# Performance work log

Measured on AMD Instinct MI355X. Metric: run time of the kernel, lower is better.

The kernel has to match this reference:

```python
import jax, jax.numpy as jnp
import numpy as np

N_TERMS = 26000
N_EDGES = 120000
BATCH = 64
N_FEAT = 14          # n_base_models + 4
GO_EMB = 8
HID = 64
IN_DIM = N_FEAT + GO_EMB  # 22


def setup_inputs() -> dict:
    key = jax.random.key(0)
    ks = jax.random.split(key, 12)
    s = 0.05
    return {
        "x": jax.random.normal(ks[0], (BATCH, N_TERMS, N_FEAT), jnp.float32),
        "edge_index": jax.random.randint(ks[1], (2, N_EDGES), 0, N_TERMS, jnp.int32),
        "term_indices": jnp.arange(N_TERMS, dtype=jnp.int32),
        "emb_table": jax.random.normal(ks[2], (N_TERMS, GO_EMB), jnp.float32),
        "W1": jax.random.normal(ks[3], (HID, IN_DIM), jnp.float32) * s,
        "b1": jnp.zeros((HID,), jnp.float32),
        "W2": jax.random.normal(ks[4], (HID, HID), jnp.float32) * s,
        "b2": jnp.zeros((HID,), jnp.float32),
        "W3": jax.random.normal(ks[5], (HID // 2, HID), jnp.float32) * s,
        "b3": jnp.zeros((HID // 2,), jnp.float32),
        "Wout": jax.random.normal(ks[6], (1, HID // 2), jnp.float32) * s,
        "bout": jnp.zeros((1,), jnp.float32),
    }


def _go_conv(x, row, col, deg_inv, W, b):
    # x: [B, N, C]. Mean-aggregate neighbor features (col -> row), add self, linear.
    agg = jnp.zeros_like(x).at[:, row].add(x[:, col])        # scatter_add over edges
    agg = agg * deg_inv[None, :, None]
    return jnp.einsum('bnc,oc->bno', x + agg, W) + b


def reference(x, edge_index, term_indices, emb_table, W1, b1, W2, b2, W3, b3, Wout, bout):
    B, N, _ = x.shape
    row, col = edge_index[0], edge_index[1]
    deg = jnp.zeros((N,), x.dtype).at[row].add(1.0)
    deg_inv = 1.0 / jnp.clip(deg, 1.0)

    go_emb = emb_table[term_indices]                          # [N, GO_EMB]
    h = jnp.concatenate([x, jnp.broadcast_to(go_emb[None], (B, N, go_emb.shape[-1]))], axis=-1)

    h = jax.nn.relu(_go_conv(h, row, col, deg_inv, W1, b1))   # dropout: eval mode (identity)
    h = jax.nn.relu(_go_conv(h, row, col, deg_inv, W2, b2))
    h = jax.nn.relu(_go_conv(h, row, col, deg_inv, W3, b3))
    out = jax.nn.sigmoid(jnp.einsum('bnc,oc->bno', h, Wout) + bout)  # [B, N, 1]
    return out[..., 0]
```

## Files before the change

### kernel.cpp

```cpp
#include <hip/hip_runtime.h>
#include <stdint.h>

static constexpr int NT = 26000;
static constexpr int NE = 120000;

typedef __attribute__((ext_vector_type(8))) short short8;
typedef __attribute__((ext_vector_type(4))) float f32x4;
typedef __attribute__((ext_vector_type(2))) unsigned int u32x2;

__device__ __forceinline__ float bf_lo(uint32_t u){ union{uint32_t u; float f;} a; a.u = u<<16; return a.f; }
__device__ __forceinline__ float bf_hi(uint32_t u){ union{uint32_t u; float f;} a; a.u = u & 0xffff0000u; return a.f; }
__device__ __forceinline__ uint32_t f2b(float f){ union{float f; uint32_t u;} a; a.f=f; return (a.u + 0x7fffu + ((a.u>>16)&1u))>>16; }

__device__ __forceinline__ void nts2(uint32_t* p, uint32_t a, uint32_t b){
  u32x2 v; v.x = a; v.y = b;
  __builtin_nontemporal_store(v, reinterpret_cast<u32x2*>(p));
}


__global__ __launch_bounds__(256) void k_zero_deg(int* __restrict__ deg){
  int i = blockIdx.x*256 + threadIdx.x;
  if (i < NT) deg[i] = 0;
}
__global__ __launch_bounds__(256) void k_count(const int* __restrict__ ei, int* __restrict__ deg){
  int e = blockIdx.x*256 + threadIdx.x;
  if (e < NE) atomicAdd(&deg[ei[e]], 1);
}
__global__ __launch_bounds__(1024) void k_scan(const int* __restrict__ deg, int* __restrict__ rp,
                                               int* __restrict__ cur){
  __shared__ int part[1024];
  const int t = threadIdx.x;
  const int CH = (NT + 1023)/1024;
  const int base = t*CH;
  int sum = 0;
  for (int i=0;i<CH;i++){
    int idx=base+i;
    if (idx<NT){ int d = deg[idx]; sum += (d<=4)?4:((d+3)&~3); }
  }
  part[t] = sum;
  __syncthreads();
  for (int off=1; off<1024; off<<=1){
    int v = (t>=off) ? part[t-off] : 0;
    __syncthreads();
    part[t] += v;
    __syncthreads();
  }
  int run = (t==0) ? 0 : part[t-1];
  for (int i=0;i<CH;i++){
    int idx = base+i;
    if (idx<NT){
      int d = deg[idx];
      int slot = (d<=4)?4:((d+3)&~3);
      rp[idx] = run; cur[idx] = run;
      run += slot;
    }
  }
  if (t==1023) rp[NT] = part[1023];
}
__global__ __launch_bounds__(256) void k_init(uint32_t* __restrict__ zp, uint32_t* __restrict__ cols32){
  int i = blockIdx.x*256 + threadIdx.x;
  if (i < 1024) zp[i] = 0;
  else if (i < 1024 + 112004) cols32[i-1024] = 0x65906590u;
}
__global__ __launch_bounds__(256) void k_fill(const int* __restrict__ ei, int* __restrict__ cur,
                                              uint16_t* __restrict__ cols){
  int e = blockIdx.x*256 + threadIdx.x;
  if (e < NE){
    int r = ei[e];
    int pos = atomicAdd(&cur[r], 1);
    cols[pos] = (uint16_t)ei[NE + e];
  }
}
__global__ __launch_bounds__(256) void k_prepw(const float* __restrict__ W1, const float* __restrict__ W2,
                                               const float* __restrict__ W3,
                                               uint16_t* __restrict__ Wt1, uint16_t* __restrict__ Wt2,
                                               uint16_t* __restrict__ Wt3){
  for (int idx = threadIdx.x; idx < 8192; idx += 256){
    if (idx < 2048){
      int o = idx >> 5, k = idx & 31;
      Wt1[idx] = (uint16_t)((k < 22) ? f2b(W1[o*22 + k]) : 0);
    } else if (idx < 6144){
      int j = idx - 2048;
      Wt2[j] = (uint16_t)f2b(W2[j]);
    } else {
      int j = idx - 6144;
      Wt3[j] = (uint16_t)f2b(W3[j]);
    }
  }
}

__global__ __launch_bounds__(256) void k_build_h0(const float* __restrict__ x, const int* __restrict__ tidx,
                                                  const float* __restrict__ emb, uint32_t* __restrict__ h0){
  const int n  = blockIdx.x*16 + (threadIdx.x & 15);
  const int b0 = threadIdx.x >> 4;
  const float* er = emb + (size_t)tidx[n]*8;
  float ev[8];
  #pragma unroll
  for (int i=0;i<8;i++) ev[i]=er[i];
  uint32_t* dst = h0 + (size_t)n*512;

  #pragma unroll
  for (int h=0; h<2; h++){
    const int b = b0 + h*16;
    const float* xr = x + ((size_t)b*NT + n)*14;
    float v[32];
    #pragma unroll
    for (int i=0;i<14;i++) v[i]=xr[i];
    #pragma unroll
    for (int i=0;i<8;i++) v[14+i]=ev[i];
    #pragma unroll
    for (int i=22;i<32;i++) v[i]=0.f;
    uint32_t p[16];
    #pragma unroll
    for (int u=0;u<16;u++) p[u] = f2b(v[2*u]) | (f2b(v[2*u+1])<<16);
    const int base = (b>>4)*256 + (b&15)*8;
    *reinterpret_cast<uint4*>(dst + base)       = make_uint4(p[0],p[1],p[2],p[3]);
    *reinterpret_cast<uint4*>(dst + base + 4)   = make_uint4(p[4],p[5],p[6],p[7]);
    *reinterpret_cast<uint4*>(dst + base + 128)     = make_uint4(p[8],p[9],p[10],p[11]);
    *reinterpret_cast<uint4*>(dst + base + 132) = make_uint4(p[12],p[13],p[14],p[15]);
  }
}

template<int STR>
__device__ __forceinline__ const uint32_t* nbp(const uint32_t* __restrict__ hin,
                                               const uint32_t* __restrict__ zp, int c){
  return (c < NT) ? (hin + (size_t)c*STR) : zp;
}
template<int KS>
__device__ __forceinline__ void gloadv(uint4 (&v)[KS], const uint32_t* __restrict__ p,
                                       const uint32_t (&off)[KS]){
  #pragma unroll
  for (int ks=0; ks<KS; ks++) v[ks] = *reinterpret_cast<const uint4*>(p + off[ks]);
}
template<int KS>
__device__ __forceinline__ void accum(float (&acc)[KS][8], const uint4 (&v)[KS]){
  #pragma unroll
  for (int ks=0;ks<KS;ks++){
    acc[ks][0]+=bf_lo(v[ks].x); acc[ks][1]+=bf_hi(v[ks].x);
    acc[ks][2]+=bf_lo(v[ks].y); acc[ks][3]+=bf_hi(v[ks].y);
    acc[ks][4]+=bf_lo(v[ks].z); acc[ks][5]+=bf_hi(v[ks].z);
    acc[ks][6]+=bf_lo(v[ks].w); acc[ks][7]+=bf_hi(v[ks].w);
  }
}

template<int KS, int STR>
__device__ __forceinline__ float aggregate(float (&acc)[KS][8],
    const uint32_t* __restrict__ hin, const uint32_t* __restrict__ zp,
    const int* __restrict__ rp, const int* __restrict__ cur,
    const uint16_t* __restrict__ cols, int node, const uint32_t (&off)[KS])
{
  const int e0 = __builtin_amdgcn_readfirstlane(rp[node]);
  const int e1 = __builtin_amdgcn_readfirstlane(rp[node+1]);
  const int dg = __builtin_amdgcn_readfirstlane(cur[node]) - e0;

  uint2 cc0 = *reinterpret_cast<const uint2*>(cols + e0);
  int q0 = __builtin_amdgcn_readfirstlane(cc0.x);
  int q1 = __builtin_amdgcn_readfirstlane(cc0.y);
  uint4 v0[KS], v1[KS], v2[KS], v3[KS], own[KS];
  gloadv<KS>(v0, nbp<STR>(hin, zp, q0 & 0xffff), off);
  gloadv<KS>(v1, nbp<STR>(hin, zp, (q0 >> 16) & 0xffff), off);
  gloadv<KS>(v2, nbp<STR>(hin, zp, q1 & 0xffff), off);
  gloadv<KS>(v3, nbp<STR>(hin, zp, (q1 >> 16) & 0xffff), off);
  gloadv<KS>(own, hin + (size_t)node*STR, off);
  uint2 ccA = *reinterpret_cast<const uint2*>(cols + e0 + 4);

  const float degf = (float)(dg > 1 ? dg : 1);
  #pragma unroll
  for (int ks=0;ks<KS;ks++){
    acc[ks][0]=bf_lo(own[ks].x)*degf; acc[ks][1]=bf_hi(own[ks].x)*degf;
    acc[ks][2]=bf_lo(own[ks].y)*degf; acc[ks][3]=bf_hi(own[ks].y)*degf;
    acc[ks][4]=bf_lo(own[ks].z)*degf; acc[ks][5]=bf_hi(own[ks].z)*degf;
    acc[ks][6]=bf_lo(own[ks].w)*degf; acc[ks][7]=bf_hi(own[ks].w)*degf;
  }

  for (int e = e0; e < e1; e += 4){
    uint2 ccN = *reinterpret_cast<const uint2*>(cols + e + 8);
    int p0 = __builtin_amdgcn_readfirstlane(ccA.x);
    int p1 = __builtin_amdgcn_readfirstlane(ccA.y);
    int n0 = (e+4 < e1) ? (p0 & 0xffff)         : NT;
    int n1 = (e+5 < e1) ? ((p0 >> 16) & 0xffff) : NT;
    int n2 = (e+6 < e1) ? (p1 & 0xffff)         : NT;
    int n3 = (e+7 < e1) ? ((p1 >> 16) & 0xffff) : NT;
    accum<KS>(acc, v0); gloadv<KS>(v0, nbp<STR>(hin, zp, n0), off);
    accum<KS>(acc, v1); gloadv<KS>(v1, nbp<STR>(hin, zp, n1), off);
    accum<KS>(acc, v2); gloadv<KS>(v2, nbp<STR>(hin, zp, n2), off);
    accum<KS>(acc, v3); gloadv<KS>(v3, nbp<STR>(hin, zp, n3), off);
    ccA = ccN;
  }
  return 1.0f / degf;
}

__global__ __launch_bounds__(256, 8) void k_layer1(
    const uint32_t* __restrict__ hin, uint32_t* __restrict__ hout,
    const int* __restrict__ rp, const int* __restrict__ cur,
    const uint16_t* __restrict__ cols, const uint32_t* __restrict__ zp,
    const uint16_t* __restrict__ Wt, const float* __restrict__ bias)
{
  constexpr int CIN=32, COUT=64, KS=1, OT=4, STR=16*CIN;
  const int t=threadIdx.x, lane=t&63, w=t>>6, l15=lane&15, lg=lane>>4;
  const int rt = w & 1;
  const int node = blockIdx.x*2 + (w>>1);

  uint32_t off[KS];
  off[0] = (uint32_t)(rt*(CIN*8) + (lg>>1)*128 + l15*8 + (lg&1)*4);

  float acc[KS][8];
  const float di = aggregate<KS,STR>(acc, hin, zp, rp, cur, cols, node, off);

  short8 bfrag[KS];
  {
    short8 bf;
    #pragma unroll
    for (int j=0;j<8;j++) bf[j] = (short)f2b(acc[0][j]*di);
    bfrag[0]=bf;
  }

  #pragma unroll
  for (int ot=0;ot<OT;ot++){
    const int o0 = ot*16;
    short8 af = *reinterpret_cast<const short8*>(Wt + (o0 + l15)*CIN + lg*8);
    f32x4 d = *reinterpret_cast<const f32x4*>(bias + o0 + lg*4);
    d = __builtin_amdgcn_mfma_f32_16x16x32_bf16(af, bfrag[0], d, 0,0,0);
    float a0=fmaxf(d[0],0.f), a1=fmaxf(d[1],0.f), a2=fmaxf(d[2],0.f), a3=fmaxf(d[3],0.f);
    nts2(hout + (size_t)node*(16*COUT) + rt*(COUT*8) + ot*128 + l15*8 + lg*2,
         f2b(a0) | (f2b(a1)<<16), f2b(a2) | (f2b(a3)<<16));
  }
}

__global__ __launch_bounds__(256, 6) void k_l2g3(
    const uint32_t* __restrict__ hin, uint32_t* __restrict__ hout,
    const int* __restrict__ rp, const int* __restrict__ cur,
    const uint16_t* __restrict__ cols, const uint32_t* __restrict__ zp,
    const uint16_t* __restrict__ Wt2, const float* __restrict__ bias,
    const uint16_t* __restrict__ Wt3)
{
  constexpr int CIN=64, COUT=64, KS=2, OT=4, STR=16*CIN;
  __shared__ uint32_t lt[4*512];

  const int t=threadIdx.x, lane=t&63, w=t>>6, l15=lane&15, lg=lane>>4;
  const int rt = w & 1;
  const int node = blockIdx.x*2 + (w>>1);

  uint32_t off[KS];
  #pragma unroll
  for (int ks=0;ks<KS;ks++)
    off[ks] = (uint32_t)(rt*(CIN*8) + (ks*2+(lg>>1))*128 + l15*8 + (lg&1)*4);

  float acc[KS][8];
  const float di = aggregate<KS,STR>(acc, hin, zp, rp, cur, cols, node, off);

  short8 bfrag[KS];
  #pragma unroll
  for (int ks=0;ks<KS;ks++){
    short8 bf;
    #pragma unroll
    for (int j=0;j<8;j++) bf[j] = (short)f2b(acc[ks][j]*di);
    bfrag[ks]=bf;
  }

  uint32_t* L = lt + w*512;
  #pragma unroll
  for (int ot=0;ot<OT;ot++){
    const int o0 = ot*16;
    short8 af0 = *reinterpret_cast<const short8*>(Wt2 + (o0 + l15)*CIN + lg*8);
    short8 af1 = *reinterpret_cast<const short8*>(Wt2 + (o0 + l15)*CIN + 32 + lg*8);
    f32x4 d = *reinterpret_cast<const f32x4*>(bias + o0 + lg*4);
    d = __builtin_amdgcn_mfma_f32_16x16x32_bf16(af0, bfrag[0], d, 0,0,0);
    d = __builtin_amdgcn_mfma_f32_16x16x32_bf16(af1, bfrag[1], d, 0,0,0);
    float a0=fmaxf(d[0],0.f), a1=fmaxf(d[1],0.f), a2=fmaxf(d[2],0.f), a3=fmaxf(d[3],0.f);
    *reinterpret_cast<uint2*>(L + ot*128 + l15*8 + lg*2) =
        make_uint2(f2b(a0) | (f2b(a1)<<16), f2b(a2) | (f2b(a3)<<16));
  }

  short8 b3f[2];
  #pragma unroll
  for (int ks=0;ks<2;ks++)
    b3f[ks] = *reinterpret_cast<const short8*>(L + (ks*2+(lg>>1))*128 + l15*8 + (lg&1)*4);

  #pragma unroll
  for (int ot=0;ot<2;ot++){
    const int o0 = ot*16;
    short8 af0 = *reinterpret_cast<const short8*>(Wt3 + (o0 + l15)*64 + lg*8);
    short8 af1 = *reinterpret_cast<const short8*>(Wt3 + (o0 + l15)*64 + 32 + lg*8);
    f32x4 d = {0.f,0.f,0.f,0.f};
    d = __builtin_amdgcn_mfma_f32_16x16x32_bf16(af0, b3f[0], d, 0,0,0);
    d = __builtin_amdgcn_mfma_f32_16x16x32_bf16(af1, b3f[1], d, 0,0,0);
    nts2(hout + (size_t)node*512 + rt*256 + ot*128 + l15*8 + lg*2,
         f2b(d[0]) | (f2b(d[1])<<16), f2b(d[2]) | (f2b(d[3])<<16));
  }
}

__global__ __launch_bounds__(256, 8) void k_fin(
    const uint32_t* __restrict__ hin,
    const int* __restrict__ rp, const int* __restrict__ cur,
    const uint16_t* __restrict__ cols, const uint32_t* __restrict__ zp,
    const float* __restrict__ b3, const float* __restrict__ Wo, const float* __restrict__ bo,
    float* __restrict__ tmp)
{
  constexpr int KS=1, STR=512;
  const int t=threadIdx.x, lane=t&63, w=t>>6, l15=lane&15, lg=lane>>4;
  const int rt = w & 1;
  const int node = blockIdx.x*2 + (w>>1);

  uint32_t off[KS];
  off[0] = (uint32_t)(rt*256 + (lg>>1)*128 + l15*8 + (lg&1)*4);

  float acc[KS][8];
  const float di = aggregate<KS,STR>(acc, hin, zp, rp, cur, cols, node, off);

  const int k0 = lg*8;
  f32x4 bA = *reinterpret_cast<const f32x4*>(b3 + k0);
  f32x4 bB = *reinterpret_cast<const f32x4*>(b3 + k0 + 4);
  f32x4 wA = *reinterpret_cast<const f32x4*>(Wo + k0);
  f32x4 wB = *reinterpret_cast<const f32x4*>(Wo + k0 + 4);
  float z = 0.f;
  #pragma unroll
  for (int j=0;j<4;j++){
    z += fmaxf(acc[0][j]  *di + bA[j], 0.f) * wA[j];
    z += fmaxf(acc[0][4+j]*di + bB[j], 0.f) * wB[j];
  }
  z += __shfl_xor(z, 16, 64);
  z += __shfl_xor(z, 32, 64);
  if (lg == 0){
    float sg = 1.f/(1.f + expf(-(z + bo[0])));
    tmp[(size_t)node*32 + rt*16 + l15] = sg;
  }
}

__global__ __launch_bounds__(256) void k_tr(const float* __restrict__ tmp, float* __restrict__ out){
  int n = blockIdx.x*256 + threadIdx.x;
  if (n < NT){
    f32x4 r[8];
    #pragma unroll
    for (int q=0;q<8;q++) r[q] = *reinterpret_cast<const f32x4*>(tmp + (size_t)n*32 + q*4);
    #pragma unroll
    for (int q=0;q<8;q++)
      #pragma unroll
      for (int j=0;j<4;j++)
        out[(size_t)(q*4+j)*NT + n] = r[q][j];
  }
}

static constexpr size_t OFF_P    = 0;
static constexpr size_t OFF_Q    = 53248000;
static constexpr size_t OFF_TMP  = 159744000;
static constexpr size_t OFF_ZP   = 163072000;
static constexpr size_t OFF_WT1  = OFF_ZP  + 4096;
static constexpr size_t OFF_WT2  = OFF_WT1 + 4096;
static constexpr size_t OFF_WT3  = OFF_WT2 + 8192;
static constexpr size_t OFF_DEG  = OFF_WT3 + 4096;
static constexpr size_t OFF_RP   = OFF_DEG + 104000;
static constexpr size_t OFF_CUR  = OFF_RP  + 104016;
static constexpr size_t OFF_COLS = OFF_CUR + 104000;
static constexpr size_t WS_NEED  = OFF_COLS + 448016;

extern "C" void kernel_launch(void* const* d_in, const int* in_sizes, int n_in,
                              void* d_out, int out_size, void* d_ws, size_t ws_size,
                              hipStream_t stream)
{
  const float* x    = (const float*)d_in[0];
  const int*   ei   = (const int*)  d_in[1];
  const int*   tidx = (const int*)  d_in[2];
  const float* emb  = (const float*)d_in[3];
  const float* W1   = (const float*)d_in[4];
  const float* b1   = (const float*)d_in[5];
  const float* W2   = (const float*)d_in[6];
  const float* b2   = (const float*)d_in[7];
  const float* W3   = (const float*)d_in[8];
  const float* b3   = (const float*)d_in[9];
  const float* Wo   = (const float*)d_in[10];
  const float* bo   = (const float*)d_in[11];
  float* out = (float*)d_out;

  if (ws_size < WS_NEED) return;

  char* ws = (char*)d_ws;
  uint32_t* P    = (uint32_t*)(ws + OFF_P);
  uint32_t* Q    = (uint32_t*)(ws + OFF_Q);
  float*    tmpf = (float*)   (ws + OFF_TMP);
  uint32_t* zp   = (uint32_t*)(ws + OFF_ZP);
  uint16_t* Wt1  = (uint16_t*)(ws + OFF_WT1);
  uint16_t* Wt2  = (uint16_t*)(ws + OFF_WT2);
  uint16_t* Wt3  = (uint16_t*)(ws + OFF_WT3);
  int*      deg  = (int*)     (ws + OFF_DEG);
  int*      rp   = (int*)     (ws + OFF_RP);
  int*      cur  = (int*)     (ws + OFF_CUR);
  uint16_t* cols = (uint16_t*)(ws + OFF_COLS);

  k_zero_deg<<<(NT+255)/256, 256, 0, stream>>>(deg);
  k_count   <<<(NE+255)/256, 256, 0, stream>>>(ei, deg);
  k_scan    <<<1, 1024, 0, stream>>>(deg, rp, cur);
  k_init    <<<442, 256, 0, stream>>>(zp, (uint32_t*)cols);
  k_fill    <<<(NE+255)/256, 256, 0, stream>>>(ei, cur, cols);
  k_prepw   <<<1, 256, 0, stream>>>(W1, W2, W3, Wt1, Wt2, Wt3);

  for (int ch = 0; ch < 2; ch++){
    k_build_h0<<<NT/16, 256, 0, stream>>>(x + (size_t)ch*32*NT*14, tidx, emb, P);
    k_layer1<<<NT/2, 256, 0, stream>>>(P, Q, rp, cur, cols, zp, Wt1, b1);
    k_l2g3  <<<NT/2, 256, 0, stream>>>(Q, P, rp, cur, cols, zp, Wt2, b2, Wt3);
    k_fin   <<<NT/2, 256, 0, stream>>>(P, rp, cur, cols, zp, b3, Wo, bo, tmpf);
    k_tr    <<<(NT+255)/256, 256, 0, stream>>>(tmpf, out + (size_t)ch*32*NT);
  }
}
```

Before: 560.4 us.

## Store intermediate layer activations as int8 with per-node-per-half scales

Layer-1 and layer-2/3 outputs are now quantized to int8, with one float scale per node and row-tile computed by a wavefront max-reduction, replacing the previous bf16 storage. The following aggregation kernels gather int8 rows and dequantize them while accumulating. This halves the bytes moved in the neighbor-gather traffic that dominates these memory-bound kernels. The cost is lower numerical precision, plus an extra scale load per neighbor and the dequantization arithmetic.

Measured after the change: 523.8 us. -6.5%, faster.

```diff
diff --git a/kernel.cpp b/kernel.cpp
--- a/kernel.cpp
+++ b/kernel.cpp
@@ -6,17 +6,12 @@
 
 typedef __attribute__((ext_vector_type(8))) short short8;
 typedef __attribute__((ext_vector_type(4))) float f32x4;
-typedef __attribute__((ext_vector_type(2))) unsigned int u32x2;
+
+__device__ __forceinline__ int rfl(int v){ return __builtin_amdgcn_readfirstlane(v); }
 
 __device__ __forceinline__ float bf_lo(uint32_t u){ union{uint32_t u; float f;} a; a.u = u<<16; return a.f; }
 __device__ __forceinline__ float bf_hi(uint32_t u){ union{uint32_t u; float f;} a; a.u = u & 0xffff0000u; return a.f; }
 __device__ __forceinline__ uint32_t f2b(float f){ union{float f; uint32_t u;} a; a.f=f; return (a.u + 0x7fffu + ((a.u>>16)&1u))>>16; }
-
-__device__ __forceinline__ void nts2(uint32_t* p, uint32_t a, uint32_t b){
-  u32x2 v; v.x = a; v.y = b;
-  __builtin_nontemporal_store(v, reinterpret_cast<u32x2*>(p));
-}
-
 
 __global__ __launch_bounds__(256) void k_zero_deg(int* __restrict__ deg){
   int i = blockIdx.x*256 + threadIdx.x;
@@ -57,10 +52,12 @@
   }
   if (t==1023) rp[NT] = part[1023];
 }
-__global__ __launch_bounds__(256) void k_init(uint32_t* __restrict__ zp, uint32_t* __restrict__ cols32){
+__global__ __launch_bounds__(256) void k_init(uint32_t* __restrict__ zp, uint32_t* __restrict__ cols32,
+                                              float* __restrict__ scQ, float* __restrict__ scY){
   int i = blockIdx.x*256 + threadIdx.x;
   if (i < 1024) zp[i] = 0;
   else if (i < 1024 + 112004) cols32[i-1024] = 0x65906590u;
+  if (i < 2){ scQ[NT*2+i] = 0.f; scY[NT*2+i] = 0.f; }
 }
 __global__ __launch_bounds__(256) void k_fill(const int* __restrict__ ei, int* __restrict__ cur,
                                               uint16_t* __restrict__ cols){
@@ -116,8 +113,8 @@
     const int base = (b>>4)*256 + (b&15)*8;
     *reinterpret_cast<uint4*>(dst + base)       = make_uint4(p[0],p[1],p[2],p[3]);
     *reinterpret_cast<uint4*>(dst + base + 4)   = make_uint4(p[4],p[5],p[6],p[7]);
-    *reinterpret_cast<uint4*>(dst + base + 128)     = make_uint4(p[8],p[9],p[10],p[11]);
-    *reinterpret_cast<uint4*>(dst + base + 132) = make_uint4(p[12],p[13],p[14],p[15]);
+    *reinterpret_cast<uint4*>(dst + base + 128)   = make_uint4(p[8],p[9],p[10],p[11]);
+    *reinterpret_cast<uint4*>(dst + base + 132)   = make_uint4(p[12],p[13],p[14],p[15]);
   }
 }
 
@@ -142,20 +139,18 @@
     acc[ks][6]+=bf_lo(v[ks].w); acc[ks][7]+=bf_hi(v[ks].w);
   }
 }
-
 template<int KS, int STR>
 __device__ __forceinline__ float aggregate(float (&acc)[KS][8],
     const uint32_t* __restrict__ hin, const uint32_t* __restrict__ zp,
     const int* __restrict__ rp, const int* __restrict__ cur,
     const uint16_t* __restrict__ cols, int node, const uint32_t (&off)[KS])
 {
-  const int e0 = __builtin_amdgcn_readfirstlane(rp[node]);
-  const int e1 = __builtin_amdgcn_readfirstlane(rp[node+1]);
-  const int dg = __builtin_amdgcn_readfirstlane(cur[node]) - e0;
+  const int e0 = rfl(rp[node]);
+  const int e1 = rfl(rp[node+1]);
+  const int dg = rfl(cur[node]) - e0;
 
   uint2 cc0 = *reinterpret_cast<const uint2*>(cols + e0);
-  int q0 = __builtin_amdgcn_readfirstlane(cc0.x);
-  int q1 = __builtin_amdgcn_readfirstlane(cc0.y);
+  int q0 = rfl(cc0.x), q1 = rfl(cc0.y);
   uint4 v0[KS], v1[KS], v2[KS], v3[KS], own[KS];
   gloadv<KS>(v0, nbp<STR>(hin, zp, q0 & 0xffff), off);
   gloadv<KS>(v1, nbp<STR>(hin, zp, (q0 >> 16) & 0xffff), off);
@@ -175,8 +170,7 @@
 
   for (int e = e0; e < e1; e += 4){
     uint2 ccN = *reinterpret_cast<const uint2*>(cols + e + 8);
-    int p0 = __builtin_amdgcn_readfirstlane(ccA.x);
-    int p1 = __builtin_amdgcn_readfirstlane(ccA.y);
+    int p0 = rfl(ccA.x), p1 = rfl(ccA.y);
     int n0 = (e+4 < e1) ? (p0 & 0xffff)         : NT;
     int n1 = (e+5 < e1) ? ((p0 >> 16) & 0xffff) : NT;
     int n2 = (e+6 < e1) ? (p1 & 0xffff)         : NT;
@@ -190,68 +184,149 @@
   return 1.0f / degf;
 }
 
+template<int KS> struct VecT;
+template<> struct VecT<2>{ using T = uint4; };
+template<> struct VecT<1>{ using T = uint2; };
+
+__device__ __forceinline__ void dqu32(float* a, uint32_t u, float s){
+  a[0] += s*(float)(int8_t)(u & 0xff);
+  a[1] += s*(float)(int8_t)((u>>8) & 0xff);
+  a[2] += s*(float)(int8_t)((u>>16) & 0xff);
+  a[3] += s*(float)(int8_t)(u>>24);
+}
+template<int KS>
+__device__ __forceinline__ void dqv(float (&acc)[KS][8], const typename VecT<KS>::T& v, float s){
+  if constexpr (KS==2){
+    dqu32(&acc[0][0], v.x, s); dqu32(&acc[0][4], v.y, s);
+    dqu32(&acc[1][0], v.z, s); dqu32(&acc[1][4], v.w, s);
+  } else {
+    dqu32(&acc[0][0], v.x, s); dqu32(&acc[0][4], v.y, s);
+  }
+}
+template<int KS, int STRB>
+__device__ __forceinline__ float aggregate_i8(float (&acc)[KS][8],
+    const uint8_t* __restrict__ hin, const uint8_t* __restrict__ zp8,
+    const float* __restrict__ sc,
+    const int* __restrict__ rp, const int* __restrict__ cur,
+    const uint16_t* __restrict__ cols, int node, uint32_t offB, int rt)
+{
+  using V = typename VecT<KS>::T;
+  const int e0 = rfl(rp[node]);
+  const int e1 = rfl(rp[node+1]);
+  const int dg = rfl(cur[node]) - e0;
+
+  uint2 cc0 = *reinterpret_cast<const uint2*>(cols + e0);
+  int a0 = rfl(cc0.x), a1 = rfl(cc0.y);
+  int c0 = a0 & 0xffff, c1 = (a0>>16) & 0xffff, c2 = a1 & 0xffff, c3 = (a1>>16) & 0xffff;
+  auto bp = [&](int c)->const uint8_t*{ return (c < NT) ? (hin + (size_t)c*STRB) : zp8; };
+
+  V v0 = *reinterpret_cast<const V*>(bp(c0) + offB); float s0 = sc[c0*2+rt];
+  V v1 = *reinterpret_cast<const V*>(bp(c1) + offB); float s1 = sc[c1*2+rt];
+  V v2 = *reinterpret_cast<const V*>(bp(c2) + offB); float s2 = sc[c2*2+rt];
+  V v3 = *reinterpret_cast<const V*>(bp(c3) + offB); float s3 = sc[c3*2+rt];
+  V ow = *reinterpret_cast<const V*>(hin + (size_t)node*STRB + offB);
+  float so = sc[node*2+rt];
+  uint2 ccA = *reinterpret_cast<const uint2*>(cols + e0 + 4);
+
+  const float degf = (float)(dg > 1 ? dg : 1);
+  #pragma unroll
+  for (int ks=0;ks<KS;ks++)
+    #pragma unroll
+    for (int j=0;j<8;j++) acc[ks][j]=0.f;
+  dqv<KS>(acc, ow, so*degf);
+
+  for (int e = e0; e < e1; e += 4){
+    uint2 ccN = *reinterpret_cast<const uint2*>(cols + e + 8);
+    int p0 = rfl(ccA.x), p1 = rfl(ccA.y);
+    int n0 = (e+4 < e1) ? (p0 & 0xffff)         : NT;
+    int n1 = (e+5 < e1) ? ((p0 >> 16) & 0xffff) : NT;
+    int n2 = (e+6 < e1) ? (p1 & 0xffff)         : NT;
+    int n3 = (e+7 < e1) ? ((p1 >> 16) & 0xffff) : NT;
+    dqv<KS>(acc, v0, s0); v0 = *reinterpret_cast<const V*>(bp(n0) + offB); s0 = sc[n0*2+rt];
+    dqv<KS>(acc, v1, s1); v1 = *reinterpret_cast<const V*>(bp(n1) + offB); s1 = sc[n1*2+rt];
+    dqv<KS>(acc, v2, s2); v2 = *reinterpret_cast<const V*>(bp(n2) + offB); s2 = sc[n2*2+rt];
+    dqv<KS>(acc, v3, s3); v3 = *reinterpret_cast<const V*>(bp(n3) + offB); s3 = sc[n3*2+rt];
+    ccA = ccN;
+  }
+  return 1.0f / degf;
+}
+
 __global__ __launch_bounds__(256, 8) void k_layer1(
-    const uint32_t* __restrict__ hin, uint32_t* __restrict__ hout,
+    const uint32_t* __restrict__ hin, uint8_t* __restrict__ qout, float* __restrict__ scQ,
     const int* __restrict__ rp, const int* __restrict__ cur,
     const uint16_t* __restrict__ cols, const uint32_t* __restrict__ zp,
     const uint16_t* __restrict__ Wt, const float* __restrict__ bias)
 {
-  constexpr int CIN=32, COUT=64, KS=1, OT=4, STR=16*CIN;
+  constexpr int CIN=32, STR=16*CIN;
   const int t=threadIdx.x, lane=t&63, w=t>>6, l15=lane&15, lg=lane>>4;
   const int rt = w & 1;
   const int node = blockIdx.x*2 + (w>>1);
 
-  uint32_t off[KS];
+  uint32_t off[1];
   off[0] = (uint32_t)(rt*(CIN*8) + (lg>>1)*128 + l15*8 + (lg&1)*4);
 
-  float acc[KS][8];
-  const float di = aggregate<KS,STR>(acc, hin, zp, rp, cur, cols, node, off);
-
-  short8 bfrag[KS];
-  {
-    short8 bf;
-    #pragma unroll
-    for (int j=0;j<8;j++) bf[j] = (short)f2b(acc[0][j]*di);
-    bfrag[0]=bf;
-  }
-
-  #pragma unroll
-  for (int ot=0;ot<OT;ot++){
+  float acc[1][8];
+  const float di = aggregate<1,STR>(acc, hin, zp, rp, cur, cols, node, off);
+
+  short8 bfrag;
+  #pragma unroll
+  for (int j=0;j<8;j++) bfrag[j] = (short)f2b(acc[0][j]*di);
+
+  float av[4][4];
+  float m = 0.f;
+  #pragma unroll
+  for (int ot=0;ot<4;ot++){
     const int o0 = ot*16;
     short8 af = *reinterpret_cast<const short8*>(Wt + (o0 + l15)*CIN + lg*8);
     f32x4 d = *reinterpret_cast<const f32x4*>(bias + o0 + lg*4);
-    d = __builtin_amdgcn_mfma_f32_16x16x32_bf16(af, bfrag[0], d, 0,0,0);
-    float a0=fmaxf(d[0],0.f), a1=fmaxf(d[1],0.f), a2=fmaxf(d[2],0.f), a3=fmaxf(d[3],0.f);
-    nts2(hout + (size_t)node*(16*COUT) + rt*(COUT*8) + ot*128 + l15*8 + lg*2,
-         f2b(a0) | (f2b(a1)<<16), f2b(a2) | (f2b(a3)<<16));
-  }
+    d = __builtin_amdgcn_mfma_f32_16x16x32_bf16(af, bfrag, d, 0,0,0);
+    #pragma unroll
+    for (int j=0;j<4;j++){
+      float v = fmaxf(d[j], 0.f);
+      av[ot][j] = v;
+      m = fmaxf(m, v);
+    }
+  }
+  #pragma unroll
+  for (int sh=1; sh<64; sh<<=1) m = fmaxf(m, __shfl_xor(m, sh, 64));
+  const float inv = (m > 0.f) ? 127.0f/m : 0.f;
+
+  uint8_t* base = qout + (size_t)node*2048 + rt*1024 + l15*64;
+  #pragma unroll
+  for (int ot=0;ot<4;ot++){
+    uint32_t pk = 0;
+    #pragma unroll
+    for (int j=0;j<4;j++){
+      int q = __float2int_rn(av[ot][j]*inv);
+      pk |= (uint32_t)(q & 0xff) << (8*j);
+    }
+    uint32_t boff = ((((ot&1)<<1)|(lg>>1))<<4) + ((ot>>1)<<3) + ((lg&1)<<2);
+    __builtin_nontemporal_store(pk, reinterpret_cast<uint32_t*>(base + boff));
+  }
+  if (lane == 0) scQ[node*2+rt] = m * (1.0f/127.0f);
 }
 
 __global__ __launch_bounds__(256, 6) void k_l2g3(
-    const uint32_t* __restrict__ hin, uint32_t* __restrict__ hout,
+    const uint8_t* __restrict__ qin, const float* __restrict__ scQ,
+    uint8_t* __restrict__ yout, float* __restrict__ scY,
     const int* __restrict__ rp, const int* __restrict__ cur,
-    const uint16_t* __restrict__ cols, const uint32_t* __restrict__ zp,
+    const uint16_t* __restrict__ cols, const uint8_t* __restrict__ zp8,
     const uint16_t* __restrict__ Wt2, const float* __restrict__ bias,
     const uint16_t* __restrict__ Wt3)
 {
-  constexpr int CIN=64, COUT=64, KS=2, OT=4, STR=16*CIN;
   __shared__ uint32_t lt[4*512];
-
   const int t=threadIdx.x, lane=t&63, w=t>>6, l15=lane&15, lg=lane>>4;
   const int rt = w & 1;
   const int node = blockIdx.x*2 + (w>>1);
 
-  uint32_t off[KS];
-  #pragma unroll
-  for (int ks=0;ks<KS;ks++)
-    off[ks] = (uint32_t)(rt*(CIN*8) + (ks*2+(lg>>1))*128 + l15*8 + (lg&1)*4);
-
-  float acc[KS][8];
-  const float di = aggregate<KS,STR>(acc, hin, zp, rp, cur, cols, node, off);
-
-  short8 bfrag[KS];
-  #pragma unroll
-  for (int ks=0;ks<KS;ks++){
+  const uint32_t offB = (uint32_t)(rt*1024 + l15*64 + lg*16);
+
+  float acc[2][8];
+  const float di = aggregate_i8<2,2048>(acc, qin, zp8, scQ, rp, cur, cols, node, offB, rt);
+
+  short8 bfrag[2];
+  #pragma unroll
+  for (int ks=0;ks<2;ks++){
     short8 bf;
     #pragma unroll
     for (int j=0;j<8;j++) bf[j] = (short)f2b(acc[ks][j]*di);
@@ -260,10 +335,10 @@
 
   uint32_t* L = lt + w*512;
   #pragma unroll
-  for (int ot=0;ot<OT;ot++){
+  for (int ot=0;ot<4;ot++){
     const int o0 = ot*16;
-    short8 af0 = *reinterpret_cast<const short8*>(Wt2 + (o0 + l15)*CIN + lg*8);
-    short8 af1 = *reinterpret_cast<const short8*>(Wt2 + (o0 + l15)*CIN + 32 + lg*8);
+    short8 af0 = *reinterpret_cast<const short8*>(Wt2 + (o0 + l15)*64 + lg*8);
+    short8 af1 = *reinterpret_cast<const short8*>(Wt2 + (o0 + l15)*64 + 32 + lg*8);
     f32x4 d = *reinterpret_cast<const f32x4*>(bias + o0 + lg*4);
     d = __builtin_amdgcn_mfma_f32_16x16x32_bf16(af0, bfrag[0], d, 0,0,0);
     d = __builtin_amdgcn_mfma_f32_16x16x32_bf16(af1, bfrag[1], d, 0,0,0);
@@ -277,6 +352,8 @@
   for (int ks=0;ks<2;ks++)
     b3f[ks] = *reinterpret_cast<const short8*>(L + (ks*2+(lg>>1))*128 + l15*8 + (lg&1)*4);
 
+  float dd[2][4];
+  float m = 0.f;
   #pragma unroll
   for (int ot=0;ot<2;ot++){
     const int o0 = ot*16;
@@ -285,28 +362,46 @@
     f32x4 d = {0.f,0.f,0.f,0.f};
     d = __builtin_amdgcn_mfma_f32_16x16x32_bf16(af0, b3f[0], d, 0,0,0);
     d = __builtin_amdgcn_mfma_f32_16x16x32_bf16(af1, b3f[1], d, 0,0,0);
-    nts2(hout + (size_t)node*512 + rt*256 + ot*128 + l15*8 + lg*2,
-         f2b(d[0]) | (f2b(d[1])<<16), f2b(d[2]) | (f2b(d[3])<<16));
-  }
+    #pragma unroll
+    for (int j=0;j<4;j++){
+      dd[ot][j] = d[j];
+      m = fmaxf(m, fabsf(d[j]));
+    }
+  }
+  #pragma unroll
+  for (int sh=1; sh<64; sh<<=1) m = fmaxf(m, __shfl_xor(m, sh, 64));
+  const float inv = (m > 0.f) ? 127.0f/m : 0.f;
+
+  uint8_t* base = yout + (size_t)node*1024 + rt*512 + l15*32;
+  #pragma unroll
+  for (int ot=0;ot<2;ot++){
+    uint32_t pk = 0;
+    #pragma unroll
+    for (int j=0;j<4;j++){
+      int q = __float2int_rn(dd[ot][j]*inv);
+      pk |= (uint32_t)(q & 0xff) << (8*j);
+    }
+    uint32_t boff = (((ot<<1)|(lg>>1))<<3) + ((lg&1)<<2);
+    __builtin_nontemporal_store(pk, reinterpret_cast<uint32_t*>(base + boff));
+  }
+  if (lane == 0) scY[node*2+rt] = m * (1.0f/127.0f);
 }
 
 __global__ __launch_bounds__(256, 8) void k_fin(
-    const uint32_t* __restrict__ hin,
+    const uint8_t* __restrict__ yin, const float* __restrict__ scY,
     const int* __restrict__ rp, const int* __restrict__ cur,
-    const uint16_t* __restrict__ cols, const uint32_t* __restrict__ zp,
+    const uint16_t* __restrict__ cols, const uint8_t* __restrict__ zp8,
     const float* __restrict__ b3, const float* __restrict__ Wo, const float* __restrict__ bo,
     float* __restrict__ tmp)
 {
-  constexpr int KS=1, STR=512;
   const int t=threadIdx.x, lane=t&63, w=t>>6, l15=lane&15, lg=lane>>4;
   const int rt = w & 1;
   const int node = blockIdx.x*2 + (w>>1);
 
-  uint32_t off[KS];
-  off[0] = (uint32_t)(rt*256 + (lg>>1)*128 + l15*8 + (lg&1)*4);
-
-  float acc[KS][8];
-  const float di = aggregate<KS,STR>(acc, hin, zp, rp, cur, cols, node, off);
+  const uint32_t offB = (uint32_t)(rt*512 + l15*32 + lg*8);
+
+  float acc[1][8];
+  const float di = aggregate_i8<1,1024>(acc, yin, zp8, scY, rp, cur, cols, node, offB, rt);
 
   const int k0 = lg*8;
   f32x4 bA = *reinterpret_cast<const f32x4*>(b3 + k0);
@@ -343,12 +438,14 @@
 
 static constexpr size_t OFF_P    = 0;
 static constexpr size_t OFF_Q    = 53248000;
-static constexpr size_t OFF_TMP  = 159744000;
-static constexpr size_t OFF_ZP   = 163072000;
+static constexpr size_t OFF_TMP  = 106496000;
+static constexpr size_t OFF_ZP   = 109824000;
 static constexpr size_t OFF_WT1  = OFF_ZP  + 4096;
 static constexpr size_t OFF_WT2  = OFF_WT1 + 4096;
 static constexpr size_t OFF_WT3  = OFF_WT2 + 8192;
-static constexpr size_t OFF_DEG  = OFF_WT3 + 4096;
+static constexpr size_t OFF_SCQ  = OFF_WT3 + 4096;
+static constexpr size_t OFF_SCY  = OFF_SCQ + 208016;
+static constexpr size_t OFF_DEG  = OFF_SCY + 208016;
 static constexpr size_t OFF_RP   = OFF_DEG + 104000;
 static constexpr size_t OFF_CUR  = OFF_RP  + 104016;
 static constexpr size_t OFF_COLS = OFF_CUR + 104000;
@@ -376,12 +473,16 @@
 
   char* ws = (char*)d_ws;
   uint32_t* P    = (uint32_t*)(ws + OFF_P);
-  uint32_t* Q    = (uint32_t*)(ws + OFF_Q);
+  uint8_t*  Y3   = (uint8_t*) (ws + OFF_P);
+  uint8_t*  Q    = (uint8_t*) (ws + OFF_Q);
   float*    tmpf = (float*)   (ws + OFF_TMP);
   uint32_t* zp   = (uint32_t*)(ws + OFF_ZP);
+  uint8_t*  zp8  = (uint8_t*) (ws + OFF_ZP);
   uint16_t* Wt1  = (uint16_t*)(ws + OFF_WT1);
   uint16_t* Wt2  = (uint16_t*)(ws + OFF_WT2);
   uint16_t* Wt3  = (uint16_t*)(ws + OFF_WT3);
+  float*    scQ  = (float*)   (ws + OFF_SCQ);
+  float*    scY  = (float*)   (ws + OFF_SCY);
   int*      deg  = (int*)     (ws + OFF_DEG);
   int*      rp   = (int*)     (ws + OFF_RP);
   int*      cur  = (int*)     (ws + OFF_CUR);
@@ -390,15 +491,15 @@
   k_zero_deg<<<(NT+255)/256, 256, 0, stream>>>(deg);
   k_count   <<<(NE+255)/256, 256, 0, stream>>>(ei, deg);
   k_scan    <<<1, 1024, 0, stream>>>(deg, rp, cur);
-  k_init    <<<442, 256, 0, stream>>>(zp, (uint32_t*)cols);
+  k_init    <<<442, 256, 0, stream>>>(zp, (uint32_t*)cols, scQ, scY);
   k_fill    <<<(NE+255)/256, 256, 0, stream>>>(ei, cur, cols);
   k_prepw   <<<1, 256, 0, stream>>>(W1, W2, W3, Wt1, Wt2, Wt3);
 
   for (int ch = 0; ch < 2; ch++){
     k_build_h0<<<NT/16, 256, 0, stream>>>(x + (size_t)ch*32*NT*14, tidx, emb, P);
-    k_layer1<<<NT/2, 256, 0, stream>>>(P, Q, rp, cur, cols, zp, Wt1, b1);
-    k_l2g3  <<<NT/2, 256, 0, stream>>>(Q, P, rp, cur, cols, zp, Wt2, b2, Wt3);
-    k_fin   <<<NT/2, 256, 0, stream>>>(P, rp, cur, cols, zp, b3, Wo, bo, tmpf);
+    k_layer1<<<NT/2, 256, 0, stream>>>(P, Q, scQ, rp, cur, cols, zp, Wt1, b1);
+    k_l2g3  <<<NT/2, 256, 0, stream>>>(Q, scQ, Y3, scY, rp, cur, cols, zp8, Wt2, b2, Wt3);
+    k_fin   <<<NT/2, 256, 0, stream>>>(Y3, scY, rp, cur, cols, zp8, b3, Wo, bo, tmpf);
     k_tr    <<<(NT+255)/256, 256, 0, stream>>>(tmpf, out + (size_t)ch*32*NT);
   }
 }
```
